# Performance work log

Hardware: AMD Instinct MI355X
Metric: run time of the kernel (lower is better)

The kernel has to match this reference:

```python
import jax, jax.numpy as jnp
import numpy as np

B, N, F, P, E, EMB = 32, 51, 4, 137, 408, 32


def _gcn_norm(edge_index, num_nodes):
    # add self loops, symmetric normalization D^-1/2 (A+I) D^-1/2 (PyG gcn_norm)
    loops = jnp.arange(num_nodes, dtype=edge_index.dtype)
    src = jnp.concatenate([edge_index[0], loops])
    dst = jnp.concatenate([edge_index[1], loops])
    w = jnp.ones(src.shape[0], dtype=jnp.float32)
    deg = jnp.zeros((num_nodes,), jnp.float32).at[dst].add(w)
    dinv = jnp.where(deg > 0, 1.0 / jnp.sqrt(deg), 0.0)
    norm = dinv[src] * w * dinv[dst]
    return src, dst, norm


def _gcn_conv(x, W, b, src, dst, norm, num_nodes):
    # x: [B, P, N, Fin] -> [B, P, N, Fout]; linear first, then normalized aggregation
    xw = jnp.einsum('bpnf,fe->bpne', x, W)
    msg = xw[:, :, src, :] * norm[None, None, :, None]
    out = jnp.zeros(xw.shape[:2] + (num_nodes, W.shape[1]), xw.dtype).at[:, :, dst, :].add(msg)
    return out + b


def _forward(x, edge_index, conv_z_w, conv_z_b, conv_r_w, conv_r_b, conv_h_w, conv_h_b,
             lin_z_w, lin_z_b, lin_r_w, lin_r_b, lin_h_w, lin_h_b, attention,
             lin1_w, lin1_b, lin2_w, lin2_b, lin3_w, lin3_b):
    num_nodes = x.shape[1]
    xt = jnp.transpose(x, (0, 3, 1, 2))  # [B, P, N, F] -- periods as a batch dim
    src, dst, norm = _gcn_norm(edge_index, num_nodes)
    # A3TGCN2 never updates H across periods (H stays None -> zeros), so all 137
    # TGCN2 cell evaluations are independent and can be vectorized over P.
    cz = _gcn_conv(xt, conv_z_w, conv_z_b, src, dst, norm, num_nodes)
    ch = _gcn_conv(xt, conv_h_w, conv_h_b, src, dst, norm, num_nodes)
    zeros_h = jnp.zeros_like(cz)
    # Z = sigmoid(lin_z([conv_z(x), H])) with H = 0
    Z = jax.nn.sigmoid(jnp.concatenate([cz, zeros_h], axis=-1) @ lin_z_w + lin_z_b)
    # R gate multiplies H (= 0) so it has no effect on the output; omitted (DCE-equivalent).
    # H_tilde = tanh(lin_h([conv_h(x), H * R])) with H = 0
    Ht = jnp.tanh(jnp.concatenate([ch, zeros_h], axis=-1) @ lin_h_w + lin_h_b)
    Hp = (1.0 - Z) * Ht  # Z*H + (1-Z)*H_tilde with H = 0 -> [B, P, N, EMB]
    probs = jax.nn.softmax(attention)
    h = jnp.einsum('p,bpne->bne', probs, Hp)  # attention-weighted accumulation
    h = jax.nn.relu(h)
    # dropout(0.2) is identity in eval mode
    h = jax.nn.relu(h @ lin1_w + lin1_b)
    h = h @ lin2_w + lin2_b            # [B, N, 1]
    h = h.reshape(-1, num_nodes)       # [B, N]
    h = jax.nn.sigmoid(h @ lin3_w + lin3_b)  # [B, 1]
    return h.reshape(-1)


def setup_inputs() -> dict:
    key = jax.random.key(0)
    ks = jax.random.split(key, 16)
    def rn(k, shape, scale=0.1):
        return jax.random.normal(k, shape, dtype=jnp.float32) * scale
    return {
        'x': jax.random.normal(ks[0], (B, N, F, P), dtype=jnp.float32),
        'edge_index': jax.random.randint(ks[1], (2, E), 0, N, dtype=jnp.int32),
        'conv_z_w': rn(ks[2], (F, EMB)), 'conv_z_b': jnp.zeros((EMB,), jnp.float32),
        'conv_r_w': rn(ks[3], (F, EMB)), 'conv_r_b': jnp.zeros((EMB,), jnp.float32),
        'conv_h_w': rn(ks[4], (F, EMB)), 'conv_h_b': jnp.zeros((EMB,), jnp.float32),
        'lin_z_w': rn(ks[5], (2 * EMB, EMB)), 'lin_z_b': jnp.zeros((EMB,), jnp.float32),
        'lin_r_w': rn(ks[6], (2 * EMB, EMB)), 'lin_r_b': jnp.zeros((EMB,), jnp.float32),
        'lin_h_w': rn(ks[7], (2 * EMB, EMB)), 'lin_h_b': jnp.zeros((EMB,), jnp.float32),
        'attention': jax.random.uniform(ks[8], (P,), dtype=jnp.float32),
        'lin1_w': rn(ks[9], (EMB, 32)), 'lin1_b': jnp.zeros((32,), jnp.float32),
        'lin2_w': rn(ks[10], (32, 1)), 'lin2_b': jnp.zeros((1,), jnp.float32),
        'lin3_w': rn(ks[11], (N, 1)), 'lin3_b': jnp.zeros((1,), jnp.float32),
    }


def reference(x, edge_index, conv_z_w, conv_z_b, conv_r_w, conv_r_b, conv_h_w, conv_h_b,
              lin_z_w, lin_z_b, lin_r_w, lin_r_b, lin_h_w, lin_h_b, attention,
              lin1_w, lin1_b, lin2_w, lin2_b, lin3_w, lin3_b):
    return _forward(x, edge_index, conv_z_w, conv_z_b, conv_r_w, conv_r_b, conv_h_w, conv_h_b,
                    lin_z_w, lin_z_b, lin_r_w, lin_r_b, lin_h_w, lin_h_b, attention,
                    lin1_w, lin1_b, lin2_w, lin2_b, lin3_w, lin3_b)
```

## Files before the change

kernel.cpp:

```cpp
#include <hip/hip_runtime.h>
#include <hip/hip_bf16.h>

#define NND 51
#define FIN 4
#define PDIM 137
#define EMB 32
#define EE 408
#define BD 32
#define PC 5
#define NCH 28
#define NE (NND*EMB)

#define WS_AMP   0
#define WS_PROBS 2608
#define WS_WU    2752
#define WS_BEFF  3008
#define WS_CNT   3072
#define WS_H     3104

#define OFF_AS   0
#define OFF_XS   2604
#define OFF_AG   3624
#define OFF_WU   4644
#define OFF_BE   4900
#define OFF_PR   4964
#define SM_N     4972

__global__ __launch_bounds__(256) void setup_kernel(
    const int* __restrict__ ei, const float* __restrict__ att,
    const float* __restrict__ Wz, const float* __restrict__ bz,
    const float* __restrict__ Wh, const float* __restrict__ bh,
    const float* __restrict__ Uz, const float* __restrict__ bz2,
    const float* __restrict__ Uh, const float* __restrict__ bh2,
    float* __restrict__ ws)
{
    int t = threadIdx.x, blk = blockIdx.x;
    if (blk > 0) {
        float4* dst = (float4*)(ws + WS_CNT);
        const int n4 = (32 + BD * NE) / 4;
        float4 z = make_float4(0.f, 0.f, 0.f, 0.f);
        for (int i = (blk - 1) * 256 + t; i < n4; i += 7 * 256) dst[i] = z;
        return;
    }
    __shared__ float deg[NND], dinv[NND];
    __shared__ float Am[2604];
    __shared__ float Us[2][EMB * EMB];
    __shared__ float Ws2[2][FIN * EMB];
    __shared__ float atts[PDIM];
    __shared__ float inv_sum;
    for (int i = t; i < 2604; i += 256) Am[i] = 0.0f;
    if (t < NND) deg[t] = 0.0f;
    for (int i = t; i < EMB * EMB; i += 256) { Us[0][i] = Uz[i]; Us[1][i] = Uh[i]; }
    if (t < FIN * EMB) { Ws2[0][t] = Wz[t]; Ws2[1][t] = Wh[t]; }
    if (t < PDIM) atts[t] = att[t];
    __syncthreads();
    for (int e = t; e < EE; e += 256) atomicAdd(&deg[ei[EE + e]], 1.0f);
    __syncthreads();
    if (t < NND) dinv[t] = rsqrtf(deg[t] + 1.0f);
    __syncthreads();
    for (int e = t; e < EE; e += 256) {
        int s = ei[e], d = ei[EE + e];
        atomicAdd(&Am[d * NND + s], dinv[s] * dinv[d]);
    }
    {
        int g = t >> 7, f = (t >> 5) & 3, e = t & 31;
        float a = 0.0f;
        for (int k = 0; k < EMB; k++) a += Ws2[g][f * EMB + k] * Us[g][k * EMB + e];
        ws[WS_WU + t] = a;
    }
    if (t < 64) {
        int g = t >> 5, e = t & 31;
        const float* bb = g ? bh : bz;
        const float* b2 = g ? bh2 : bz2;
        float a = b2[e];
        for (int k = 0; k < EMB; k++) a += bb[k] * Us[g][k * EMB + e];
        ws[WS_BEFF + t] = a;
    }
    __syncthreads();
    if (t < NND) Am[t * 52] += dinv[t] * dinv[t];
    if (t == 0) {
        float m = -1e30f;
        for (int p = 0; p < PDIM; p++) m = fmaxf(m, atts[p]);
        float s = 0.0f;
        for (int p = 0; p < PDIM; p++) { float v = __expf(atts[p] - m); atts[p] = v; s += v; }
        inv_sum = 1.0f / s;
    }
    __syncthreads();
    for (int i = t; i < 2604; i += 256) ws[WS_AMP + i] = Am[i];
    if (t < PDIM) ws[WS_PROBS + t] = atts[t] * inv_sum;
}

__global__ __launch_bounds__(256) void main_kernel(
    const float* __restrict__ x, const float* __restrict__ ws,
    float* __restrict__ h)
{
    __shared__ __align__(16) float sm[SM_N];
    int t = threadIdx.x;
    int b = blockIdx.y;
    int c = blockIdx.x;
    int p0 = c * PC;
    int npp = min(PC, PDIM - p0);

    for (int i = t; i < 651; i += 256)
        ((float4*)(sm + OFF_AS))[i] = ((const float4*)(ws + WS_AMP))[i];
    sm[OFF_WU + t] = ws[WS_WU + t];
    if (t < 64) sm[OFF_BE + t] = ws[WS_BEFF + t];
    if (t < npp) sm[OFF_PR + t] = ws[WS_PROBS + p0 + t];
    if (t < NND * FIN) {
        int n = t >> 2, f = t & 3;
        const float* xp = &x[((b * NND + n) * FIN + f) * PDIM + p0];
        for (int pp = 0; pp < npp; pp++) sm[OFF_XS + (pp * NND + n) * 4 + f] = xp[pp];
    }
    __syncthreads();

    int e = t & 31, r = t >> 5;
    float wuz[4], wuh[4];
    #pragma unroll
    for (int f = 0; f < 4; f++) {
        wuz[f] = sm[OFF_WU + f * EMB + e];
        wuh[f] = sm[OFF_WU + 128 + f * EMB + e];
    }
    float bez = sm[OFF_BE + e], beh = sm[OFF_BE + 32 + e];

    if (t < NND * PC) {
        int pp = t / NND, d = t - pp * NND;
        if (pp < npp) {
            const float*  Ad = sm + OFF_AS + d * NND;
            const float4* xr = (const float4*)(sm + OFF_XS) + pp * NND;
            float4 acc = make_float4(0.f, 0.f, 0.f, 0.f);
            #pragma unroll 3
            for (int s = 0; s < NND; s++) {
                float a = Ad[s]; float4 xv = xr[s];
                acc.x += a * xv.x; acc.y += a * xv.y;
                acc.z += a * xv.z; acc.w += a * xv.w;
            }
            ((float4*)(sm + OFF_AG))[pp * NND + d] = acc;
        }
    }
    __syncthreads();

    float hacc[7] = {0, 0, 0, 0, 0, 0, 0};
    for (int pp = 0; pp < npp; pp++) {
        float pr = sm[OFF_PR + pp];
        #pragma unroll
        for (int k = 0; k < 7; k++) {
            int d = r + 8 * k;
            if (d < NND) {
                float4 ag = ((const float4*)(sm + OFF_AG))[pp * NND + d];
                float az = bez + ag.x * wuz[0] + ag.y * wuz[1] + ag.z * wuz[2] + ag.w * wuz[3];
                float ah = beh + ag.x * wuh[0] + ag.y * wuh[1] + ag.z * wuh[2] + ag.w * wuh[3];
                float Z  = 1.0f / (1.0f + __expf(-az));
                float Ht = 2.0f / (1.0f + __expf(-2.0f * ah)) - 1.0f;
                hacc[k] += pr * (1.0f - Z) * Ht;
            }
        }
    }
    float* dst = &h[b * NE];
    #pragma unroll
    for (int k = 0; k < 7; k++) {
        int d = r + 8 * k;
        if (d < NND) atomicAdd(&dst[d * EMB + e], hacc[k]);
    }
}

__global__ __launch_bounds__(256) void head_kernel(
    const float* __restrict__ h, const float* __restrict__ W1,
    const float* __restrict__ b1, const float* __restrict__ w2,
    const float* __restrict__ b2, const float* __restrict__ w3,
    const float* __restrict__ b3, float* __restrict__ out)
{
    __shared__ float hs[NE];
    __shared__ float W1s[EMB * EMB];
    __shared__ float b1s[EMB], w2s[EMB];
    __shared__ float w3s[NND];
    __shared__ float wsum[4];
    int t = threadIdx.x, b = blockIdx.x;
    for (int i = t; i < NE; i += 256) hs[i] = fmaxf(h[b * NE + i], 0.0f);
    for (int i = t; i < EMB * EMB; i += 256) W1s[i] = W1[i];
    if (t < EMB) { b1s[t] = b1[t]; w2s[t] = w2[t]; }
    if (t < NND) w3s[t] = w3[t];
    __syncthreads();
    float acc = 0.0f;
    for (int i = t; i < NE; i += 256) {
        int d = i >> 5, e = i & 31;
        float a = b1s[e];
        const float* hr = &hs[d * EMB];
        #pragma unroll
        for (int k = 0; k < EMB; k++) a += hr[k] * W1s[k * EMB + e];
        a = fmaxf(a, 0.0f);
        acc += w3s[d] * w2s[e] * a;
    }
    #pragma unroll
    for (int off = 32; off > 0; off >>= 1) acc += __shfl_down(acc, off);
    if ((t & 63) == 0) wsum[t >> 6] = acc;
    __syncthreads();
    if (t == 0) {
        float s = wsum[0] + wsum[1] + wsum[2] + wsum[3];
        float s3 = 0.0f;
        for (int d = 0; d < NND; d++) s3 += w3s[d];
        float v = s + b2[0] * s3 + b3[0];
        out[b] = 1.0f / (1.0f + __expf(-v));
    }
}

extern "C" void kernel_launch(void* const* d_in, const int* in_sizes, int n_in,
                              void* d_out, int out_size, void* d_ws, size_t ws_size,
                              hipStream_t stream) {
    const float* x         = (const float*)d_in[0];
    const int*   ei        = (const int*)d_in[1];
    const float* conv_z_w  = (const float*)d_in[2];
    const float* conv_z_b  = (const float*)d_in[3];
    const float* conv_h_w  = (const float*)d_in[6];
    const float* conv_h_b  = (const float*)d_in[7];
    const float* lin_z_w   = (const float*)d_in[8];
    const float* lin_z_b   = (const float*)d_in[9];
    const float* lin_h_w   = (const float*)d_in[12];
    const float* lin_h_b   = (const float*)d_in[13];
    const float* attention = (const float*)d_in[14];
    const float* lin1_w    = (const float*)d_in[15];
    const float* lin1_b    = (const float*)d_in[16];
    const float* lin2_w    = (const float*)d_in[17];
    const float* lin2_b    = (const float*)d_in[18];
    const float* lin3_w    = (const float*)d_in[19];
    const float* lin3_b    = (const float*)d_in[20];

    float* ws = (float*)d_ws;
    float* h  = ws + WS_H;

    hipLaunchKernelGGL(setup_kernel, dim3(8), dim3(256), 0, stream,
                       ei, attention, conv_z_w, conv_z_b, conv_h_w, conv_h_b,
                       lin_z_w, lin_z_b, lin_h_w, lin_h_b, ws);
    hipLaunchKernelGGL(main_kernel, dim3(NCH, BD), dim3(256), 0, stream,
                       x, ws, h);
    hipLaunchKernelGGL(head_kernel, dim3(BD), dim3(256), 0, stream,
                       h, lin1_w, lin1_b, lin2_w, lin2_b, lin3_w, lin3_b,
                       (float*)d_out);
}
```

Before: 130.0 us.

## Fuse setup into main kernel and replace atomics with per-chunk slab reduction

Removes the separate setup kernel by having every main_kernel block recompute the normalized adjacency, fused weights and softmax probabilities in shared memory. Global atomicAdd accumulation into h is replaced by plain stores into a per-(batch, chunk) slab, which the head kernel then sums over 28 chunks. This saves one kernel launch plus the zeroing pass and avoids atomic contention. In exchange, 896 blocks each redo the setup work, and the head kernel reads 28x more data.

Measured after the change: 142.3 us. +9.5%, slower.

```diff
diff --git a/kernel.cpp b/kernel.cpp
--- a/kernel.cpp
+++ b/kernel.cpp
@@ -11,122 +11,100 @@
 #define NCH 28
 #define NE (NND*EMB)
 
-#define WS_AMP   0
-#define WS_PROBS 2608
-#define WS_WU    2752
-#define WS_BEFF  3008
-#define WS_CNT   3072
-#define WS_H     3104
-
-#define OFF_AS   0
-#define OFF_XS   2604
-#define OFF_AG   3624
-#define OFF_WU   4644
-#define OFF_BE   4900
-#define OFF_PR   4964
-#define SM_N     4972
-
-__global__ __launch_bounds__(256) void setup_kernel(
-    const int* __restrict__ ei, const float* __restrict__ att,
+#define WS_SLAB 0
+
+__global__ __launch_bounds__(256) void main_kernel(
+    const float* __restrict__ x, const int* __restrict__ ei,
+    const float* __restrict__ att,
     const float* __restrict__ Wz, const float* __restrict__ bz,
     const float* __restrict__ Wh, const float* __restrict__ bh,
     const float* __restrict__ Uz, const float* __restrict__ bz2,
     const float* __restrict__ Uh, const float* __restrict__ bh2,
-    float* __restrict__ ws)
+    float* __restrict__ slab)
 {
-    int t = threadIdx.x, blk = blockIdx.x;
-    if (blk > 0) {
-        float4* dst = (float4*)(ws + WS_CNT);
-        const int n4 = (32 + BD * NE) / 4;
-        float4 z = make_float4(0.f, 0.f, 0.f, 0.f);
-        for (int i = (blk - 1) * 256 + t; i < n4; i += 7 * 256) dst[i] = z;
-        return;
-    }
-    __shared__ float deg[NND], dinv[NND];
-    __shared__ float Am[2604];
+    __shared__ __align__(16) float Am[2604];
+    __shared__ __align__(16) float xs[PC * NND * FIN];
+    __shared__ __align__(16) float ag[PC * NND * FIN];
     __shared__ float Us[2][EMB * EMB];
     __shared__ float Ws2[2][FIN * EMB];
-    __shared__ float atts[PDIM];
-    __shared__ float inv_sum;
-    for (int i = t; i < 2604; i += 256) Am[i] = 0.0f;
-    if (t < NND) deg[t] = 0.0f;
-    for (int i = t; i < EMB * EMB; i += 256) { Us[0][i] = Uz[i]; Us[1][i] = Uh[i]; }
-    if (t < FIN * EMB) { Ws2[0][t] = Wz[t]; Ws2[1][t] = Wh[t]; }
-    if (t < PDIM) atts[t] = att[t];
-    __syncthreads();
-    for (int e = t; e < EE; e += 256) atomicAdd(&deg[ei[EE + e]], 1.0f);
-    __syncthreads();
-    if (t < NND) dinv[t] = rsqrtf(deg[t] + 1.0f);
-    __syncthreads();
-    for (int e = t; e < EE; e += 256) {
-        int s = ei[e], d = ei[EE + e];
-        atomicAdd(&Am[d * NND + s], dinv[s] * dinv[d]);
-    }
-    {
-        int g = t >> 7, f = (t >> 5) & 3, e = t & 31;
-        float a = 0.0f;
-        for (int k = 0; k < EMB; k++) a += Ws2[g][f * EMB + k] * Us[g][k * EMB + e];
-        ws[WS_WU + t] = a;
-    }
-    if (t < 64) {
-        int g = t >> 5, e = t & 31;
-        const float* bb = g ? bh : bz;
-        const float* b2 = g ? bh2 : bz2;
-        float a = b2[e];
-        for (int k = 0; k < EMB; k++) a += bb[k] * Us[g][k * EMB + e];
-        ws[WS_BEFF + t] = a;
-    }
-    __syncthreads();
-    if (t < NND) Am[t * 52] += dinv[t] * dinv[t];
-    if (t == 0) {
-        float m = -1e30f;
-        for (int p = 0; p < PDIM; p++) m = fmaxf(m, atts[p]);
-        float s = 0.0f;
-        for (int p = 0; p < PDIM; p++) { float v = __expf(atts[p] - m); atts[p] = v; s += v; }
-        inv_sum = 1.0f / s;
-    }
-    __syncthreads();
-    for (int i = t; i < 2604; i += 256) ws[WS_AMP + i] = Am[i];
-    if (t < PDIM) ws[WS_PROBS + t] = atts[t] * inv_sum;
-}
-
-__global__ __launch_bounds__(256) void main_kernel(
-    const float* __restrict__ x, const float* __restrict__ ws,
-    float* __restrict__ h)
-{
-    __shared__ __align__(16) float sm[SM_N];
+    __shared__ float wu[2 * FIN * EMB];
+    __shared__ float beff[64];
+    __shared__ float deg[NND], dinv[NND];
+    __shared__ float atts[PDIM], pr[PC];
+    __shared__ float smax, sinv;
+    __shared__ int   eis[2 * EE];
+
     int t = threadIdx.x;
     int b = blockIdx.y;
     int c = blockIdx.x;
     int p0 = c * PC;
     int npp = min(PC, PDIM - p0);
 
-    for (int i = t; i < 651; i += 256)
-        ((float4*)(sm + OFF_AS))[i] = ((const float4*)(ws + WS_AMP))[i];
-    sm[OFF_WU + t] = ws[WS_WU + t];
-    if (t < 64) sm[OFF_BE + t] = ws[WS_BEFF + t];
-    if (t < npp) sm[OFF_PR + t] = ws[WS_PROBS + p0 + t];
+    for (int i = t; i < 2604; i += 256) Am[i] = 0.0f;
+    if (t < NND) deg[t] = 0.0f;
+    for (int i = t; i < 2 * EE; i += 256) eis[i] = ei[i];
+    for (int i = t; i < EMB * EMB; i += 256) { Us[0][i] = Uz[i]; Us[1][i] = Uh[i]; }
+    if (t < FIN * EMB) { Ws2[0][t] = Wz[t]; Ws2[1][t] = Wh[t]; }
+    if (t < PDIM) atts[t] = att[t];
     if (t < NND * FIN) {
         int n = t >> 2, f = t & 3;
         const float* xp = &x[((b * NND + n) * FIN + f) * PDIM + p0];
-        for (int pp = 0; pp < npp; pp++) sm[OFF_XS + (pp * NND + n) * 4 + f] = xp[pp];
-    }
-    __syncthreads();
-
-    int e = t & 31, r = t >> 5;
-    float wuz[4], wuh[4];
-    #pragma unroll
-    for (int f = 0; f < 4; f++) {
-        wuz[f] = sm[OFF_WU + f * EMB + e];
-        wuh[f] = sm[OFF_WU + 128 + f * EMB + e];
-    }
-    float bez = sm[OFF_BE + e], beh = sm[OFF_BE + 32 + e];
+        for (int pp = 0; pp < npp; pp++) xs[(pp * NND + n) * 4 + f] = xp[pp];
+    }
+    __syncthreads();
+
+    for (int e = t; e < EE; e += 256) atomicAdd(&deg[eis[EE + e]], 1.0f);
+    if (t >= 192) {
+        float m = -1e30f;
+        for (int p = t - 192; p < PDIM; p += 64) m = fmaxf(m, atts[p]);
+        #pragma unroll
+        for (int off = 32; off > 0; off >>= 1) m = fmaxf(m, __shfl_down(m, off));
+        if (t == 192) smax = m;
+    }
+    __syncthreads();
+
+    if (t < NND) dinv[t] = rsqrtf(deg[t] + 1.0f);
+    if (t >= 64 && t < 64 + PDIM) atts[t - 64] = __expf(atts[t - 64] - smax);
+    __syncthreads();
+
+    for (int e = t; e < EE; e += 256) {
+        int s = eis[e], d = eis[EE + e];
+        atomicAdd(&Am[d * NND + s], dinv[s] * dinv[d]);
+    }
+    {
+        int g = t >> 7, f = (t >> 5) & 3, e2 = t & 31;
+        float a = 0.0f;
+        #pragma unroll
+        for (int k = 0; k < EMB; k++) a += Ws2[g][f * EMB + k] * Us[g][k * EMB + e2];
+        wu[t] = a;
+    }
+    if (t < 64) {
+        int g = t >> 5, e2 = t & 31;
+        const float* bb = g ? bh : bz;
+        const float* b2 = g ? bh2 : bz2;
+        float a = b2[e2];
+        #pragma unroll
+        for (int k = 0; k < EMB; k++) a += bb[k] * Us[g][k * EMB + e2];
+        beff[t] = a;
+    }
+    if (t >= 192) {
+        float s = 0.0f;
+        for (int p = t - 192; p < PDIM; p += 64) s += atts[p];
+        #pragma unroll
+        for (int off = 32; off > 0; off >>= 1) s += __shfl_down(s, off);
+        if (t == 192) sinv = 1.0f / s;
+    }
+    __syncthreads();
+
+    if (t < NND) Am[t * 52] += dinv[t] * dinv[t];
+    if (t < npp) pr[t] = atts[p0 + t] * sinv;
+    __syncthreads();
 
     if (t < NND * PC) {
         int pp = t / NND, d = t - pp * NND;
         if (pp < npp) {
-            const float*  Ad = sm + OFF_AS + d * NND;
-            const float4* xr = (const float4*)(sm + OFF_XS) + pp * NND;
+            const float*  Ad = Am + d * NND;
+            const float4* xr = (const float4*)xs + pp * NND;
             float4 acc = make_float4(0.f, 0.f, 0.f, 0.f);
             #pragma unroll 3
             for (int s = 0; s < NND; s++) {
@@ -134,52 +112,73 @@
                 acc.x += a * xv.x; acc.y += a * xv.y;
                 acc.z += a * xv.z; acc.w += a * xv.w;
             }
-            ((float4*)(sm + OFF_AG))[pp * NND + d] = acc;
+            ((float4*)ag)[pp * NND + d] = acc;
         }
     }
     __syncthreads();
+
+    int e = t & 31, r = t >> 5;
+    float wuz[4], wuh[4];
+    #pragma unroll
+    for (int f = 0; f < 4; f++) {
+        wuz[f] = wu[f * EMB + e];
+        wuh[f] = wu[128 + f * EMB + e];
+    }
+    float bez = beff[e], beh = beff[32 + e];
 
     float hacc[7] = {0, 0, 0, 0, 0, 0, 0};
     for (int pp = 0; pp < npp; pp++) {
-        float pr = sm[OFF_PR + pp];
+        float p = pr[pp];
         #pragma unroll
         for (int k = 0; k < 7; k++) {
             int d = r + 8 * k;
             if (d < NND) {
-                float4 ag = ((const float4*)(sm + OFF_AG))[pp * NND + d];
-                float az = bez + ag.x * wuz[0] + ag.y * wuz[1] + ag.z * wuz[2] + ag.w * wuz[3];
-                float ah = beh + ag.x * wuh[0] + ag.y * wuh[1] + ag.z * wuh[2] + ag.w * wuh[3];
+                float4 agv = ((const float4*)ag)[pp * NND + d];
+                float az = bez + agv.x * wuz[0] + agv.y * wuz[1] + agv.z * wuz[2] + agv.w * wuz[3];
+                float ah = beh + agv.x * wuh[0] + agv.y * wuh[1] + agv.z * wuh[2] + agv.w * wuh[3];
                 float Z  = 1.0f / (1.0f + __expf(-az));
                 float Ht = 2.0f / (1.0f + __expf(-2.0f * ah)) - 1.0f;
-                hacc[k] += pr * (1.0f - Z) * Ht;
+                hacc[k] += p * (1.0f - Z) * Ht;
             }
         }
     }
-    float* dst = &h[b * NE];
+    float* dst = &slab[((size_t)b * NCH + c) * NE];
     #pragma unroll
     for (int k = 0; k < 7; k++) {
         int d = r + 8 * k;
-        if (d < NND) atomicAdd(&dst[d * EMB + e], hacc[k]);
+        if (d < NND) dst[d * EMB + e] = hacc[k];
     }
 }
 
 __global__ __launch_bounds__(256) void head_kernel(
-    const float* __restrict__ h, const float* __restrict__ W1,
+    const float* __restrict__ slab, const float* __restrict__ W1,
     const float* __restrict__ b1, const float* __restrict__ w2,
     const float* __restrict__ b2, const float* __restrict__ w3,
     const float* __restrict__ b3, float* __restrict__ out)
 {
-    __shared__ float hs[NE];
+    __shared__ __align__(16) float hs[NE];
     __shared__ float W1s[EMB * EMB];
     __shared__ float b1s[EMB], w2s[EMB];
     __shared__ float w3s[NND];
     __shared__ float wsum[4];
     int t = threadIdx.x, b = blockIdx.x;
-    for (int i = t; i < NE; i += 256) hs[i] = fmaxf(h[b * NE + i], 0.0f);
+
+    const float4* sl = (const float4*)(slab + (size_t)b * NCH * NE);
+    for (int i = t; i < NE / 4; i += 256) {
+        float4 a = sl[i];
+        #pragma unroll 4
+        for (int c2 = 1; c2 < NCH; c2++) {
+            float4 v = sl[c2 * (NE / 4) + i];
+            a.x += v.x; a.y += v.y; a.z += v.z; a.w += v.w;
+        }
+        ((float4*)hs)[i] = make_float4(fmaxf(a.x, 0.f), fmaxf(a.y, 0.f),
+                                       fmaxf(a.z, 0.f), fmaxf(a.w, 0.f));
+    }
     for (int i = t; i < EMB * EMB; i += 256) W1s[i] = W1[i];
     if (t < EMB) { b1s[t] = b1[t]; w2s[t] = w2[t]; }
     if (t < NND) w3s[t] = w3[t];
     __syncthreads();
+
     float acc = 0.0f;
     for (int i = t; i < NE; i += 256) {
         int d = i >> 5, e = i & 31;
@@ -224,15 +223,12 @@
     const float* lin3_w    = (const float*)d_in[19];
     const float* lin3_b    = (const float*)d_in[20];
 
-    float* ws = (float*)d_ws;
-    float* h  = ws + WS_H;
-
-    hipLaunchKernelGGL(setup_kernel, dim3(8), dim3(256), 0, stream,
-                       ei, attention, conv_z_w, conv_z_b, conv_h_w, conv_h_b,
-                       lin_z_w, lin_z_b, lin_h_w, lin_h_b, ws);
+    float* slab = (float*)d_ws + WS_SLAB;
+
     hipLaunchKernelGGL(main_kernel, dim3(NCH, BD), dim3(256), 0, stream,
-                       x, ws, h);
+                       x, ei, attention, conv_z_w, conv_z_b, conv_h_w, conv_h_b,
+                       lin_z_w, lin_z_b, lin_h_w, lin_h_b, slab);
     hipLaunchKernelGGL(head_kernel, dim3(BD), dim3(256), 0, stream,
-                       h, lin1_w, lin1_b, lin2_w, lin2_b, lin3_w, lin3_b,
+                       slab, lin1_w, lin1_b, lin2_w, lin2_b, lin3_w, lin3_b,
                        (float*)d_out);
 }
```

## Replace atomic accumulation with per-chunk partial slabs reduced in head kernel

Applied to the files above, without the earlier changes.

Each main_kernel block now writes its attention-weighted partial sums to its own slab with plain stores instead of atomically adding into a shared h buffer. The head kernel then sums the 28 chunk slabs per batch with float4 loads before the ReLU and MLP. This removes the zero-fill of h in setup (setup shrinks to one block) and avoids atomic contention. The cost is a larger workspace and more global reads in the head kernel, which runs on only 32 blocks. It also adds unroll pragmas to two small setup loops.

New measurement: 142.7 us. +9.8%, slower.

```diff
diff --git a/kernel.cpp b/kernel.cpp
--- a/kernel.cpp
+++ b/kernel.cpp
@@ -15,8 +15,7 @@
 #define WS_PROBS 2608
 #define WS_WU    2752
 #define WS_BEFF  3008
-#define WS_CNT   3072
-#define WS_H     3104
+#define WS_SLAB  3072
 
 #define OFF_AS   0
 #define OFF_XS   2604
@@ -34,14 +33,7 @@
     const float* __restrict__ Uh, const float* __restrict__ bh2,
     float* __restrict__ ws)
 {
-    int t = threadIdx.x, blk = blockIdx.x;
-    if (blk > 0) {
-        float4* dst = (float4*)(ws + WS_CNT);
-        const int n4 = (32 + BD * NE) / 4;
-        float4 z = make_float4(0.f, 0.f, 0.f, 0.f);
-        for (int i = (blk - 1) * 256 + t; i < n4; i += 7 * 256) dst[i] = z;
-        return;
-    }
+    int t = threadIdx.x;
     __shared__ float deg[NND], dinv[NND];
     __shared__ float Am[2604];
     __shared__ float Us[2][EMB * EMB];
@@ -65,6 +57,7 @@
     {
         int g = t >> 7, f = (t >> 5) & 3, e = t & 31;
         float a = 0.0f;
+        #pragma unroll
         for (int k = 0; k < EMB; k++) a += Ws2[g][f * EMB + k] * Us[g][k * EMB + e];
         ws[WS_WU + t] = a;
     }
@@ -73,6 +66,7 @@
         const float* bb = g ? bh : bz;
         const float* b2 = g ? bh2 : bz2;
         float a = b2[e];
+        #pragma unroll
         for (int k = 0; k < EMB; k++) a += bb[k] * Us[g][k * EMB + e];
         ws[WS_BEFF + t] = a;
     }
@@ -92,7 +86,7 @@
 
 __global__ __launch_bounds__(256) void main_kernel(
     const float* __restrict__ x, const float* __restrict__ ws,
-    float* __restrict__ h)
+    float* __restrict__ slab)
 {
     __shared__ __align__(16) float sm[SM_N];
     int t = threadIdx.x;
@@ -155,27 +149,38 @@
             }
         }
     }
-    float* dst = &h[b * NE];
+    float* dst = &slab[((size_t)b * NCH + c) * NE];
     #pragma unroll
     for (int k = 0; k < 7; k++) {
         int d = r + 8 * k;
-        if (d < NND) atomicAdd(&dst[d * EMB + e], hacc[k]);
+        if (d < NND) dst[d * EMB + e] = hacc[k];
     }
 }
 
 __global__ __launch_bounds__(256) void head_kernel(
-    const float* __restrict__ h, const float* __restrict__ W1,
+    const float* __restrict__ slab, const float* __restrict__ W1,
     const float* __restrict__ b1, const float* __restrict__ w2,
     const float* __restrict__ b2, const float* __restrict__ w3,
     const float* __restrict__ b3, float* __restrict__ out)
 {
-    __shared__ float hs[NE];
+    __shared__ __align__(16) float hs[NE];
     __shared__ float W1s[EMB * EMB];
     __shared__ float b1s[EMB], w2s[EMB];
     __shared__ float w3s[NND];
     __shared__ float wsum[4];
     int t = threadIdx.x, b = blockIdx.x;
-    for (int i = t; i < NE; i += 256) hs[i] = fmaxf(h[b * NE + i], 0.0f);
+
+    const float4* sl = (const float4*)(slab + (size_t)b * NCH * NE);
+    for (int i = t; i < NE / 4; i += 256) {
+        float4 a = sl[i];
+        #pragma unroll 4
+        for (int c2 = 1; c2 < NCH; c2++) {
+            float4 v = sl[c2 * (NE / 4) + i];
+            a.x += v.x; a.y += v.y; a.z += v.z; a.w += v.w;
+        }
+        ((float4*)hs)[i] = make_float4(fmaxf(a.x, 0.f), fmaxf(a.y, 0.f),
+                                       fmaxf(a.z, 0.f), fmaxf(a.w, 0.f));
+    }
     for (int i = t; i < EMB * EMB; i += 256) W1s[i] = W1[i];
     if (t < EMB) { b1s[t] = b1[t]; w2s[t] = w2[t]; }
     if (t < NND) w3s[t] = w3[t];
@@ -224,15 +229,15 @@
     const float* lin3_w    = (const float*)d_in[19];
     const float* lin3_b    = (const float*)d_in[20];
 
-    float* ws = (float*)d_ws;
-    float* h  = ws + WS_H;
-
-    hipLaunchKernelGGL(setup_kernel, dim3(8), dim3(256), 0, stream,
+    float* ws   = (float*)d_ws;
+    float* slab = ws + WS_SLAB;
+
+    hipLaunchKernelGGL(setup_kernel, dim3(1), dim3(256), 0, stream,
                        ei, attention, conv_z_w, conv_z_b, conv_h_w, conv_h_b,
                        lin_z_w, lin_z_b, lin_h_w, lin_h_b, ws);
     hipLaunchKernelGGL(main_kernel, dim3(NCH, BD), dim3(256), 0, stream,
-                       x, ws, h);
+                       x, ws, slab);
     hipLaunchKernelGGL(head_kernel, dim3(BD), dim3(256), 0, stream,
-                       h, lin1_w, lin1_b, lin2_w, lin2_b, lin3_w, lin3_b,
+                       slab, lin1_w, lin1_b, lin2_w, lin2_b, lin3_w, lin3_b,
                        (float*)d_out);
 }
```
